# Kernel tuning notes

Measured on AMD Instinct MI355X. Metric: run time of the kernel, lower is better.

The kernel has to match this reference:

```python
import jax, jax.numpy as jnp
import numpy as np

# Straight-through-estimator round (round_pass in the original code)
def _round_ste(x):
    return x + jax.lax.stop_gradient(jnp.round(x) - x)

INPUT_QMAX = 127.0   # 2**(input_bit-1)-1,  input_bit=8
WEIGHT_QMAX = 127.0  # 2**(weight_bit-1)-1, weight_bit=8
OUT_RANGE = 127.0    # 2**(output_bit-1)-1, output_bit=8


def setup_inputs() -> dict:
    key = jax.random.key(0)
    k0, k1, k2 = jax.random.split(key, 3)
    B, Cin, Cout, H, W, K = 16, 320, 320, 64, 64, 3
    x = jax.random.normal(k0, (B, Cin, H, W), dtype=jnp.float32)
    weight = jax.random.normal(k1, (Cout, Cin, K, K), dtype=jnp.float32) * 0.05
    bias = jax.random.normal(k2, (Cout,), dtype=jnp.float32) * 0.1
    # LSQ learned scalar step sizes (cloned from conv_lsq in the original)
    step_x = jnp.float32(0.02)
    step_w = jnp.float32(0.002)
    step_b = jnp.float32(0.01)
    # Bit_shift_layer scale: shift conv accumulator down into output_bit range
    shift_scale = jnp.float32(2.0 ** -7)
    return {"x": x, "weight": weight, "bias": bias, "step_x": step_x,
            "step_w": step_w, "step_b": step_b, "shift_scale": shift_scale}


def reference(x, weight, bias, step_x, step_w, step_b, shift_scale):
    # --- lsq_quant_input (isint=True): x_int in [-127,127], x_scale = 1/step ---
    x_int = jnp.clip(_round_ste(x / step_x), -INPUT_QMAX, INPUT_QMAX)
    x_scale = 1.0 / step_x
    # --- lsq_quant_weight (isint=True) ---
    w_int = jnp.clip(_round_ste(weight / step_w), -WEIGHT_QMAX, WEIGHT_QMAX)
    w_scale = 1.0 / step_w
    # --- Conv2d_int: integer-valued conv (no bias) ---
    y_int = jax.lax.conv_general_dilated(
        x_int, w_int, window_strides=(1, 1), padding=((1, 1), (1, 1)),
        dimension_numbers=("NCHW", "OIHW", "NCHW"))
    # --- mvm_result_shift: bit-shift accumulator into output range ---
    y_shift = jnp.clip(_round_ste(y_int * shift_scale), -OUT_RANGE, OUT_RANGE)
    # --- lsq_quant_bias (isint=False): dequantized bias ---
    b_deq = jnp.clip(_round_ste(bias / step_b), -OUT_RANGE, OUT_RANGE) * step_b
    # --- bias requant to output int scale, add, clamp (fused epilogue) ---
    b_int8 = jnp.clip(_round_ste(b_deq * shift_scale * x_scale * w_scale),
                      -OUT_RANGE, OUT_RANGE)
    y_shift_dmac = jnp.clip(y_shift + b_int8[None, :, None, None],
                            -OUT_RANGE, OUT_RANGE)
    # module returns y_shift_DMAC (the integer-valued clamped output)
    return y_shift_dmac
```

## Files before the change

kernel.cpp:

```cpp
#include <hip/hip_runtime.h>

typedef int v4i __attribute__((ext_vector_type(4)));

#define QMAX 127.0f

#define XQ_BYTES 22302720
#define WQ_BYTES 921600

__device__ __forceinline__ float clampf(float v, float lo, float hi) {
    return fminf(fmaxf(v, lo), hi);
}

__device__ __forceinline__ float qround(float v, float step, float inv) {
    float t = v * inv;
    float r = rintf(t);
    float d = fabsf(t - r);
    if (fabsf(d - 0.5f) < fabsf(t) * 1e-5f + 1e-5f)
        r = rintf(v / step);
    return r;
}

__device__ __forceinline__ void gload_lds16(const char* g, char* l) {
    __builtin_amdgcn_global_load_lds(
        (const __attribute__((address_space(1))) void*)g,
        (__attribute__((address_space(3))) void*)l, 16, 0, 0);
}

__device__ __forceinline__ v4i mfma_i8(v4i a, v4i b, v4i c) {
    return __builtin_amdgcn_mfma_i32_16x16x64_i8(a, b, c, 0, 0, 0);
}

__global__ __launch_bounds__(256) void fused_prep_kernel(
    const float* __restrict__ x, const float* __restrict__ w,
    const float* __restrict__ bias,
    const float* __restrict__ step_x_p, const float* __restrict__ step_w_p,
    const float* __restrict__ step_b_p, const float* __restrict__ shift_p,
    char* __restrict__ xq, char* __restrict__ wq2, float* __restrict__ bi)
{
    __shared__ float F[64 * 65];
    const int bid = blockIdx.x;
    const int t = threadIdx.x;

    if (bid < 1024) {
        const int h = bid & 63;
        const int b = bid >> 6;
        const float step = *step_x_p;
        const float inv  = 1.0f / step;
        const int wcol = t >> 2;
        const int cg   = t & 3;
        v4i vals[5];

        for (int c5 = 0; c5 < 5; ++c5) {
            {
                const int r = t >> 4, c = (t & 15) * 4;
                const float* src = x + (((size_t)(b * 320 + c5 * 64) * 64 + h) * 64);
#pragma unroll
                for (int i = 0; i < 4; ++i) {
                    const int row = r + i * 16;
                    *(float4*)&F[row * 65 + c] =
                        *(const float4*)(src + (size_t)row * 4096 + c);
                }
            }
            __syncthreads();
            int dws[4];
#pragma unroll
            for (int j = 0; j < 4; ++j) {
                int word = 0;
#pragma unroll
                for (int k = 0; k < 4; ++k) {
                    float v = F[(cg * 16 + j * 4 + k) * 65 + wcol];
                    int xi = (int)clampf(qround(v, step, inv), -QMAX, QMAX);
                    word |= (xi & 0xFF) << (8 * k);
                }
                dws[j] = word;
            }
            vals[c5] = (v4i){dws[0], dws[1], dws[2], dws[3]};
            __syncthreads();
        }

        const int col = wcol + 1;
        const int key = (col >> 1) & 3;
        char* base = xq + ((size_t)(b * 66 + (h + 1)) * 66 + col) * 320;
#pragma unroll
        for (int c5 = 0; c5 < 5; ++c5)
            *(v4i*)(base + c5 * 64 + (((cg ^ key)) << 4)) = vals[c5];

    } else if (bid < 4624) {
        const int tid = (bid - 1024) * 256 + t;
        const float step = *step_w_p;
        const float inv  = 1.0f / step;
        const int p    = tid / 102400;
        const int r    = tid - p * 102400;
        const int c5   = r / 20480;
        const int r2   = r - c5 * 20480;
        const int cog  = r2 >> 10;
        const int r3   = r2 & 1023;
        const int lane = r3 >> 4, j = r3 & 15;
        const int co = cog * 16 + (lane & 15);
        const int ci = c5 * 64 + (lane >> 4) * 16 + j;
        float v = w[(size_t)co * 2880 + ci * 9 + p];
        int q = (int)clampf(qround(v, step, inv), -QMAX, QMAX);
        wq2[tid] = (char)q;
    } else if (bid < 4949) {
        int tid = (bid - 4624) * 256 + t;
        if (tid < 83200) {
            int b = tid / 5200;
            int r = tid - b * 5200;
            int px = r / 20;
            int ck = (r - px * 20) * 16;
            int row, col;
            if (px < 66)       { row = 0;  col = px; }
            else if (px < 132) { row = 65; col = px - 66; }
            else { int e = px - 132; row = 1 + (e >> 1); col = (e & 1) * 65; }
            size_t off = ((size_t)(b * 66 + row) * 66 + col) * 320 + ck;
            v4i z = {0, 0, 0, 0};
            *(v4i*)&xq[off] = z;
        }
    } else {
        const float step_b = *step_b_p;
        const float xs = 1.0f / *step_x_p;
        const float ws = 1.0f / *step_w_p;
        const float shift = *shift_p;
#pragma unroll
        for (int co = t; co < 320; co += 256) {
            float b_deq = clampf(rintf(bias[co] / step_b), -QMAX, QMAX) * step_b;
            float v = ((b_deq * shift) * xs) * ws;
            bi[co] = clampf(rintf(v), -QMAX, QMAX);
        }
    }
}

__global__ __launch_bounds__(256, 3) void conv_mfma_kernel(
    const char* __restrict__ xq, const char* __restrict__ wq2,
    const float* __restrict__ bi, const float* __restrict__ shift_p,
    float* __restrict__ out)
{
    __shared__ __attribute__((aligned(16))) char B_lds[2][25344];

    const int t  = threadIdx.x;
    const int id = blockIdx.x;
    const int g  = id / 40;
    const int r  = id - g * 40;
    const int bx = r >> 3;
    const int ptile = (g << 3) | (r & 7);

    const int co0 = bx * 64;
    const int b  = ptile >> 4;
    const int h0 = (ptile & 15) * 4;

    const int wave = t >> 6, lane = t & 63;
    const int quad = lane >> 4, l15 = lane & 15;

    const char* xbase = xq + ((size_t)(b * 66 + h0) * 66) * 320;

    v4i acc[4][4] = {};

    for (int c = t; c < 1584; c += 256) {
        const char* gp = xbase + (c >> 2) * 320 + ((c & 3) << 4);
        gload_lds16(gp, &B_lds[0][(c - lane) * 16]);
    }
    __syncthreads();

    for (int c5 = 0; c5 < 5; ++c5) {
        if (c5 < 4) {
            const int ci0 = (c5 + 1) * 64;
            char* dst = B_lds[(c5 + 1) & 1];
            for (int c = t; c < 1584; c += 256) {
                const char* gp = xbase + (c >> 2) * 320 + ci0 + ((c & 3) << 4);
                gload_lds16(gp, &dst[(c - lane) * 16]);
            }
        }

        const char* Bc = B_lds[c5 & 1];
        const char* wp = wq2 + (c5 * 20 + bx * 4) * 1024 + lane * 16;

        v4i areg[2][4];
#pragma unroll
        for (int cs = 0; cs < 4; ++cs)
            areg[0][cs] = *(const v4i*)(wp + 0 * 102400 + cs * 1024);

#pragma unroll
        for (int p = 0; p < 9; ++p) {
            const int dh = p / 3, dw = p - dh * 3;
            if (p < 8) {
#pragma unroll
                for (int cs = 0; cs < 4; ++cs)
                    areg[(p + 1) & 1][cs] =
                        *(const v4i*)(wp + (p + 1) * 102400 + cs * 1024);
            }
            const int prow = wave + dh;
            auto bread = [&](int i) -> v4i {
                const int col = i * 16 + l15 + dw;
                const int key = (col >> 1) & 3;
                return *(const v4i*)&Bc[(prow * 66 + col) * 64 +
                                        ((quad ^ key) << 4)];
            };
            v4i bf = bread(0);
#pragma unroll
            for (int i = 0; i < 4; ++i) {
                v4i bcur = bf;
                if (i < 3) bf = bread(i + 1);
                __builtin_amdgcn_s_setprio(1);
#pragma unroll
                for (int cs = 0; cs < 4; ++cs)
                    acc[cs][i] = mfma_i8(areg[p & 1][cs], bcur, acc[cs][i]);
                __builtin_amdgcn_s_setprio(0);
            }
        }
        __syncthreads();
    }

    const float shift = *shift_p;
    const int h = h0 + wave;
#pragma unroll
    for (int cs = 0; cs < 4; ++cs) {
#pragma unroll
        for (int reg = 0; reg < 4; ++reg) {
            const int co = co0 + cs * 16 + quad * 4 + reg;
            const float bv = bi[co];
            float* orow = out + (((size_t)(b * 320 + co) * 64) + h) * 64;
#pragma unroll
            for (int i = 0; i < 4; ++i) {
                float y  = (float)acc[cs][i][reg];
                float ys = clampf(rintf(y * shift), -QMAX, QMAX);
                orow[i * 16 + l15] = clampf(ys + bv, -QMAX, QMAX);
            }
        }
    }
}

extern "C" void kernel_launch(void* const* d_in, const int* in_sizes, int n_in,
                              void* d_out, int out_size, void* d_ws, size_t ws_size,
                              hipStream_t stream) {
    const float* x      = (const float*)d_in[0];
    const float* w      = (const float*)d_in[1];
    const float* bias   = (const float*)d_in[2];
    const float* step_x = (const float*)d_in[3];
    const float* step_w = (const float*)d_in[4];
    const float* step_b = (const float*)d_in[5];
    const float* shift  = (const float*)d_in[6];
    float* out = (float*)d_out;

    char*  xq  = (char*)d_ws;
    char*  wq2 = xq + XQ_BYTES;
    float* bi  = (float*)(wq2 + WQ_BYTES);

    fused_prep_kernel<<<4950, 256, 0, stream>>>(x, w, bias, step_x, step_w,
                                                step_b, shift, xq, wq2, bi);
    conv_mfma_kernel<<<1280, 256, 0, stream>>>(xq, wq2, bi, shift, out);
}
```

Before: 209.8 us.

## Process two batch tiles per conv block and pack weight quantization four per thread

The conv kernel now computes two output tiles per block, for batch b and b+8, and launches 640 blocks instead of 1280. While the first tile's epilogue runs, the block is already staging the second tile's input channels into LDS. This removes the partial second wave of blocks and hides the load latency at the tile boundary, at the cost of longer-lived blocks and less scheduling flexibility. Separately, weight quantization packs four int8 values per thread with one 32-bit store, cutting the prep grid from 4950 to 2250 blocks.

```diff
diff --git a/kernel.cpp b/kernel.cpp
--- a/kernel.cpp
+++ b/kernel.cpp
@@ -85,8 +85,9 @@
         for (int c5 = 0; c5 < 5; ++c5)
             *(v4i*)(base + c5 * 64 + (((cg ^ key)) << 4)) = vals[c5];
 
-    } else if (bid < 4624) {
-        const int tid = (bid - 1024) * 256 + t;
+    } else if (bid < 1924) {
+        const int t4  = (bid - 1024) * 256 + t;
+        const int tid = t4 * 4;
         const float step = *step_w_p;
         const float inv  = 1.0f / step;
         const int p    = tid / 102400;
@@ -95,14 +96,19 @@
         const int r2   = r - c5 * 20480;
         const int cog  = r2 >> 10;
         const int r3   = r2 & 1023;
-        const int lane = r3 >> 4, j = r3 & 15;
-        const int co = cog * 16 + (lane & 15);
-        const int ci = c5 * 64 + (lane >> 4) * 16 + j;
-        float v = w[(size_t)co * 2880 + ci * 9 + p];
-        int q = (int)clampf(qround(v, step, inv), -QMAX, QMAX);
-        wq2[tid] = (char)q;
-    } else if (bid < 4949) {
-        int tid = (bid - 4624) * 256 + t;
+        const int lane = r3 >> 4, j0 = r3 & 15;
+        const int co  = cog * 16 + (lane & 15);
+        const int ci0 = c5 * 64 + (lane >> 4) * 16 + j0;
+        const float* wsrc = w + (size_t)co * 2880 + ci0 * 9 + p;
+        int word = 0;
+#pragma unroll
+        for (int k = 0; k < 4; ++k) {
+            int q = (int)clampf(qround(wsrc[k * 9], step, inv), -QMAX, QMAX);
+            word |= (q & 0xFF) << (8 * k);
+        }
+        *(int*)(wq2 + tid) = word;
+    } else if (bid < 2249) {
+        int tid = (bid - 1924) * 256 + t;
         if (tid < 83200) {
             int b = tid / 5200;
             int r = tid - b * 5200;
@@ -145,40 +151,32 @@
     const int ptile = (g << 3) | (r & 7);
 
     const int co0 = bx * 64;
-    const int b  = ptile >> 4;
+    const int b0 = ptile >> 4;
     const int h0 = (ptile & 15) * 4;
 
     const int wave = t >> 6, lane = t & 63;
     const int quad = lane >> 4, l15 = lane & 15;
 
-    const char* xbase = xq + ((size_t)(b * 66 + h0) * 66) * 320;
+    const char* xbase0 = xq + ((size_t)(b0 * 66 + h0) * 66) * 320;
+    const char* xbase1 = xq + ((size_t)((b0 + 8) * 66 + h0) * 66) * 320;
+
+    const float shift = *shift_p;
 
     v4i acc[4][4] = {};
 
-    for (int c = t; c < 1584; c += 256) {
-        const char* gp = xbase + (c >> 2) * 320 + ((c & 3) << 4);
-        gload_lds16(gp, &B_lds[0][(c - lane) * 16]);
-    }
-    __syncthreads();
-
-    for (int c5 = 0; c5 < 5; ++c5) {
-        if (c5 < 4) {
-            const int ci0 = (c5 + 1) * 64;
-            char* dst = B_lds[(c5 + 1) & 1];
-            for (int c = t; c < 1584; c += 256) {
-                const char* gp = xbase + (c >> 2) * 320 + ci0 + ((c & 3) << 4);
-                gload_lds16(gp, &dst[(c - lane) * 16]);
-            }
-        }
-
-        const char* Bc = B_lds[c5 & 1];
+    auto stage = [&](const char* xb, int ci0, char* dst) {
+        for (int c = t; c < 1584; c += 256) {
+            const char* gp = xb + (c >> 2) * 320 + ci0 + ((c & 3) << 4);
+            gload_lds16(gp, &dst[(c - lane) * 16]);
+        }
+    };
+
+    auto compute_c5 = [&](int c5, const char* Bc) {
         const char* wp = wq2 + (c5 * 20 + bx * 4) * 1024 + lane * 16;
-
         v4i areg[2][4];
 #pragma unroll
         for (int cs = 0; cs < 4; ++cs)
-            areg[0][cs] = *(const v4i*)(wp + 0 * 102400 + cs * 1024);
-
+            areg[0][cs] = *(const v4i*)(wp + cs * 1024);
 #pragma unroll
         for (int p = 0; p < 9; ++p) {
             const int dh = p / 3, dw = p - dh * 3;
@@ -207,26 +205,52 @@
                 __builtin_amdgcn_s_setprio(0);
             }
         }
+    };
+
+    auto epilogue = [&](int b) {
+        const int h = h0 + wave;
+#pragma unroll
+        for (int cs = 0; cs < 4; ++cs) {
+#pragma unroll
+            for (int reg = 0; reg < 4; ++reg) {
+                const int co = co0 + cs * 16 + quad * 4 + reg;
+                const float bv = bi[co];
+                float* orow = out + (((size_t)(b * 320 + co) * 64) + h) * 64;
+#pragma unroll
+                for (int i = 0; i < 4; ++i) {
+                    float y  = (float)acc[cs][i][reg];
+                    float ys = clampf(rintf(y * shift), -QMAX, QMAX);
+                    orow[i * 16 + l15] = clampf(ys + bv, -QMAX, QMAX);
+                }
+            }
+        }
+    };
+
+    stage(xbase0, 0, B_lds[0]);
+    __syncthreads();
+
+    for (int c5 = 0; c5 < 5; ++c5) {
+        if (c5 < 4) stage(xbase0, (c5 + 1) * 64, B_lds[(c5 + 1) & 1]);
+        else        stage(xbase1, 0,             B_lds[1]);
+        compute_c5(c5, B_lds[c5 & 1]);
         __syncthreads();
     }
 
-    const float shift = *shift_p;
-    const int h = h0 + wave;
-#pragma unroll
-    for (int cs = 0; cs < 4; ++cs) {
-#pragma unroll
-        for (int reg = 0; reg < 4; ++reg) {
-            const int co = co0 + cs * 16 + quad * 4 + reg;
-            const float bv = bi[co];
-            float* orow = out + (((size_t)(b * 320 + co) * 64) + h) * 64;
-#pragma unroll
-            for (int i = 0; i < 4; ++i) {
-                float y  = (float)acc[cs][i][reg];
-                float ys = clampf(rintf(y * shift), -QMAX, QMAX);
-                orow[i * 16 + l15] = clampf(ys + bv, -QMAX, QMAX);
-            }
-        }
+    stage(xbase1, 64, B_lds[0]);
+    epilogue(b0);
+
+#pragma unroll
+    for (int cs = 0; cs < 4; ++cs)
+#pragma unroll
+        for (int i = 0; i < 4; ++i)
+            acc[cs][i] = (v4i){0, 0, 0, 0};
+
+    for (int c5 = 0; c5 < 5; ++c5) {
+        if (c5 >= 1 && c5 < 4) stage(xbase1, (c5 + 1) * 64, B_lds[c5 & 1]);
+        compute_c5(c5, B_lds[(c5 + 1) & 1]);
+        if (c5 < 4) __syncthreads();
     }
+    epilogue(b0 + 8);
 }
 
 extern "C" void kernel_launch(void* const* d_in, const int* in_sizes, int n_in,
@@ -245,7 +269,7 @@
     char*  wq2 = xq + XQ_BYTES;
     float* bi  = (float*)(wq2 + WQ_BYTES);
 
-    fused_prep_kernel<<<4950, 256, 0, stream>>>(x, w, bias, step_x, step_w,
+    fused_prep_kernel<<<2250, 256, 0, stream>>>(x, w, bias, step_x, step_w,
                                                 step_b, shift, xq, wq2, bi);
-    conv_mfma_kernel<<<1280, 256, 0, stream>>>(xq, wq2, bi, shift, out);
-}
+    conv_mfma_kernel<<<640, 256, 0, stream>>>(xq, wq2, bi, shift, out);
+}
```

After: 227.4 us. 8.4% more time.
